# Optimization experiments

Hardware: AMD Instinct MI355X
Metric: run time of the kernel (lower is better)

Reference implementation:

```python
import jax, jax.numpy as jnp
import numpy as np

B, NPTS = 2, 60000
NX, NY = 256, 256
PCR0, PCR1 = -32.0, -32.0
PS0, PS1 = 0.25, 0.25
MAXPP = 32      # max points per pillar
MAXP = 12000    # max pillars
C = 64          # lidar_channels
SENT = NX * NY  # sentinel pillar id (> any valid id)
NEG = -1e9
EPS = 1e-5


def setup_inputs():
    key = jax.random.key(0)
    ks = jax.random.split(key, 16)
    xy = jax.random.uniform(ks[0], (B, NPTS, 2), minval=-34.0, maxval=34.0)
    z = jax.random.uniform(ks[1], (B, NPTS, 1), minval=-3.0, maxval=1.0)
    ir = jax.random.uniform(ks[2], (B, NPTS, 2))
    pts = jnp.concatenate([xy, z, ir], axis=-1).astype(jnp.float32)
    mask = jax.random.uniform(ks[3], (B, NPTS)) < 0.98

    def lin(k, i, o):
        return (jax.random.normal(k, (i, o)) / np.sqrt(i)).astype(jnp.float32)

    inp = {"lidar_points": pts, "lidar_mask": mask,
           "w1": lin(ks[4], 10, 64), "b1": 0.01 * jax.random.normal(ks[5], (64,), jnp.float32),
           "g1": jnp.ones(64, jnp.float32), "be1": jnp.zeros(64, jnp.float32),
           "w2": lin(ks[6], 64, 64), "b2": 0.01 * jax.random.normal(ks[7], (64,), jnp.float32),
           "g2": jnp.ones(64, jnp.float32), "be2": jnp.zeros(64, jnp.float32)}
    for i, n in enumerate(["1", "2", "3"]):
        inp["cw" + n] = (jax.random.normal(ks[8 + i], (64, 64, 3, 3)) / np.sqrt(64 * 9)).astype(jnp.float32)
        inp["cb" + n] = 0.01 * jax.random.normal(ks[11 + i], (64,), jnp.float32)
        inp["cg" + n] = jnp.ones(64, jnp.float32)
        inp["cbe" + n] = jnp.zeros(64, jnp.float32)
    return inp


def bn1d(x, g, b):  # training-mode BN over rows (biased var), matches torch BatchNorm1d forward
    m = x.mean(0)
    v = ((x - m) ** 2).mean(0)
    return (x - m) * jax.lax.rsqrt(v + EPS) * g + b


def bn2d(x, g, b):  # training-mode BN over (N,H,W) per channel
    m = x.mean((0, 2, 3), keepdims=True)
    v = ((x - m) ** 2).mean((0, 2, 3), keepdims=True)
    return (x - m) * jax.lax.rsqrt(v + EPS) * g[None, :, None, None] + b[None, :, None, None]


def conv3(x, w, b):
    y = jax.lax.conv_general_dilated(x, w, (1, 1), 'SAME',
                                     dimension_numbers=('NCHW', 'OIHW', 'NCHW'))
    return y + b[None, :, None, None]


def pillarize(pts, msk):
    """pts: (N,5) xyzir, msk: (N,) bool -> padded pillar tensors (fixed shapes)."""
    n = pts.shape[0]
    ix = jnp.clip(((pts[:, 0] - PCR0) / PS0).astype(jnp.int32), 0, NX - 1)
    iy = jnp.clip(((pts[:, 1] - PCR1) / PS1).astype(jnp.int32), 0, NY - 1)
    pid = jnp.where(msk, iy * NX + ix, SENT)
    # sorted unique ids; keep the first (smallest) MAXP, like torch.unique + truncation
    spid = jnp.sort(pid)
    is_new = jnp.concatenate([jnp.array([True]), spid[1:] != spid[:-1]])
    urank = jnp.cumsum(is_new) - 1
    dest = jnp.where(is_new & (urank < MAXP) & (spid < SENT), urank, MAXP)
    uids = jnp.full((MAXP + 1,), SENT, dtype=pid.dtype).at[dest].set(spid)[:MAXP]  # ascending, SENT-padded
    inv = jnp.clip(jnp.searchsorted(uids, pid), 0, MAXP - 1)
    valid = (uids[inv] == pid) & (pid < SENT)
    # rank of each point within its pillar, in original point order (stable sort)
    seg = jnp.where(valid, inv, MAXP)
    order = jnp.argsort(seg)  # stable
    sseg = seg[order]
    pos = jnp.arange(n)
    first = jnp.concatenate([jnp.array([True]), sseg[1:] != sseg[:-1]])
    start = jax.lax.cummax(jnp.where(first, pos, 0))
    rank = jnp.zeros(n, jnp.int32).at[order].set((pos - start).astype(jnp.int32))
    keep = valid & (rank < MAXPP)  # first MAXPP points per pillar (matches truncation-then-mean)
    seg2 = jnp.where(keep, inv, MAXP)  # dump slot = MAXP
    cnt = jnp.zeros(MAXP + 1, pts.dtype).at[seg2].add(1.0)
    sums = jnp.zeros((MAXP + 1, 3), pts.dtype).at[seg2].add(jnp.where(keep[:, None], pts[:, :3], 0.0))
    mean = sums / jnp.maximum(cnt, 1.0)[:, None]
    ctr = mean[seg2]  # per-point pillar centroid (over kept points)
    gx = PCR0 + ((pid % NX).astype(pts.dtype) + 0.5) * PS0
    gy = PCR1 + ((pid // NX).astype(pts.dtype) + 0.5) * PS1
    aug = jnp.concatenate([pts, pts[:, :3] - ctr, gx[:, None], gy[:, None]], axis=1)  # (N,10)
    rk = jnp.minimum(rank, MAXPP - 1)
    pf = jnp.zeros((MAXP + 1, MAXPP, 10), pts.dtype).at[seg2, rk].set(
        jnp.where(keep[:, None], aug, 0.0))[:MAXP]
    pm = jnp.zeros((MAXP + 1, MAXPP), bool).at[seg2, rk].set(keep)[:MAXP]
    pvalid = uids < SENT
    coords = jnp.where(pvalid[:, None], jnp.stack([uids % NX, uids // NX], axis=-1), 0)
    return pf, pm, coords, pvalid


def pillar_net(pf, pm, w1, b1, g1, be1, w2, b2, g2, be2):
    npil, pp, ci = pf.shape
    x = pf.reshape(npil * pp, ci) @ w1 + b1
    x = jax.nn.relu(bn1d(x, g1, be1))
    x = x @ w2 + b2
    x = jax.nn.relu(bn1d(x, g2, be2))
    x = x.reshape(npil, pp, -1)
    x = jnp.where(pm[:, :, None], x, NEG)
    return x.max(axis=1)  # (npil, C)


def reference(lidar_points, lidar_mask, w1, b1, g1, be1, w2, b2, g2, be2,
              cw1, cb1, cg1, cbe1, cw2, cb2, cg2, cbe2, cw3, cb3, cg3, cbe3):
    pf, pm, coords, pvalid = jax.vmap(pillarize)(lidar_points, lidar_mask)
    # pillar net is applied per batch element in the original loop -> per-sample BN stats
    feat = jax.vmap(lambda a, m: pillar_net(a, m, w1, b1, g1, be1, w2, b2, g2, be2))(pf, pm)
    lin = coords[..., 1] * NX + coords[..., 0]          # (B, MAXP)
    f = jnp.where(pvalid[..., None], feat, 0.0)          # padded pillars contribute nothing
    bev = jax.vmap(lambda l, ff: jnp.zeros((NY * NX, C), ff.dtype).at[l].add(ff))(lin, f)
    bev = bev.reshape(-1, NY, NX, C).transpose(0, 3, 1, 2)  # (B,C,NY,NX)
    x = jax.nn.relu(bn2d(conv3(bev, cw1, cb1), cg1, cbe1))
    x = jax.nn.relu(bn2d(conv3(x, cw2, cb2), cg2, cbe2))
    x = jax.nn.relu(bn2d(conv3(x, cw3, cb3), cg3, cbe3))
    return x
```

## Files before the change

### kernel.cpp

```cpp
#include <hip/hip_runtime.h>

#define NPTS 60000
#define NXG 256
#define NCELL 65536
#define MAXP 12000
#define MAXPP 32
#define NROWS (MAXP*MAXPP)

typedef float f32x32 __attribute__((ext_vector_type(32)));
typedef float f32x4  __attribute__((ext_vector_type(4)));
typedef short s16x8  __attribute__((ext_vector_type(8)));

__device__ __forceinline__ short to_bf16(float f){
  unsigned u = __float_as_uint(f);
  unsigned r = (u + 0x7FFFu + ((u>>16)&1u)) >> 16;
  return (short)r;
}

__global__ __launch_bounds__(256) void prep(uint4* __restrict__ p1, size_t n1,
                                            uint4* __restrict__ p2, size_t n2,
                                            const float* __restrict__ w0, const float* __restrict__ w1,
                                            const float* __restrict__ w2, short* __restrict__ wh,
                                            const float* __restrict__ mw1, const float* __restrict__ mw2,
                                            short* __restrict__ w1h, short* __restrict__ w2h){
  size_t idx = (size_t)blockIdx.x*256 + threadIdx.x;
  size_t stride = (size_t)gridDim.x*256;
  const uint4 z = make_uint4(0,0,0,0);
  for (size_t k=idx; k<n1; k+=stride) p1[k]=z;
  for (size_t k=idx; k<n2; k+=stride) p2[k]=z;
  for (size_t k=idx; k<3*36864; k+=stride){
    int l = (int)(k / 36864), r = (int)(k - (size_t)l*36864);
    const float* w = (l==0)? w0 : ((l==1)? w1 : w2);
    int ic = r & 63, oc = (r>>6)&63, tap = r>>12;
    wh[k] = to_bf16(w[(oc*64+ic)*9 + tap]);
  }
  for (size_t k=idx; k<2048; k+=stride){
    int kk = (int)(k>>6), oc = (int)(k&63);
    w1h[k] = (kk<10) ? to_bf16(mw1[kk*64+oc]) : (short)0;
  }
  for (size_t k=idx; k<4096; k+=stride)
    w2h[k] = to_bf16(mw2[k]);
}

__global__ void compute_pid(const float* __restrict__ pts, const void* __restrict__ maskp,
                            int* __restrict__ pid, int* __restrict__ pptr,
                            int* __restrict__ ccnt){
  __shared__ int cf32, cbig;
  if (threadIdx.x==0){ cf32=0; cbig=0; }
  __syncthreads();
  {
    int lf=0, lb=0;
    const unsigned* mu = (const unsigned*)maskp;
    for (int k=0;k<4;k++){
      unsigned x = mu[threadIdx.x*4+k];
      if (x==0x3f800000u) lf++;
      else if (x>1u) lb++;
    }
    if (lf) atomicAdd(&cf32, lf);
    if (lb) atomicAdd(&cbig, lb);
  }
  __syncthreads();
  int mode = (cf32>64) ? 2 : ((cbig>0) ? 1 : 0);
  int i = blockIdx.x*blockDim.x + threadIdx.x;
  if (i>=NPTS) return;
  int b = blockIdx.y;
  int gi = b*NPTS+i;
  bool m;
  if (mode==0)      m = ((const int*)maskp)[gi]!=0;
  else if (mode==1) m = ((const unsigned char*)maskp)[gi]!=0;
  else              m = ((const float*)maskp)[gi]!=0.f;
  int cell = -1;
  if (m){
    float x = pts[(size_t)gi*5+0], y = pts[(size_t)gi*5+1];
    int ix = (int)((x - (-32.0f)) / 0.25f);
    ix = ix<0?0:(ix>255?255:ix);
    int iy = (int)((y - (-32.0f)) / 0.25f);
    iy = iy<0?0:(iy>255?255:iy);
    cell = iy*NXG + ix;
    atomicAdd(&ccnt[b*NCELL+cell], 1);
  }
  pid[gi] = cell;
  pptr[gi] = -1;
}

__global__ __launch_bounds__(256) void scan_a(const int* __restrict__ ccnt,
                                              int2* __restrict__ bpart){
  int b = blockIdx.y, blk = blockIdx.x, t = threadIdx.x;
  int4 v = *(const int4*)&ccnt[b*NCELL + blk*1024 + t*4];
  int occ = (v.x>0)+(v.y>0)+(v.z>0)+(v.w>0);
  int cnt = v.x+v.y+v.z+v.w;
  #pragma unroll
  for (int off=32; off>0; off>>=1){
    occ += __shfl_xor(occ, off, 64);
    cnt += __shfl_xor(cnt, off, 64);
  }
  __shared__ int so[4], sc[4];
  int wv = t>>6, lane = t&63;
  if (lane==0){ so[wv]=occ; sc[wv]=cnt; }
  __syncthreads();
  if (t==0) bpart[b*64+blk] = make_int2(so[0]+so[1]+so[2]+so[3], sc[0]+sc[1]+sc[2]+sc[3]);
}

__global__ __launch_bounds__(256) void scan_b(const int* __restrict__ ccnt,
    const int2* __restrict__ bpart,
    int* __restrict__ crank, int* __restrict__ cstart, int* __restrict__ pcell,
    int* __restrict__ misc, int* __restrict__ heavy){
  __shared__ int swo[4], swc[4], sk[4];
  __shared__ int bo_, bc_;
  int b = blockIdx.y, blk = blockIdx.x, t = threadIdx.x;
  int wv = t>>6, lane = t&63;
  if (t < 64){
    int2 p = bpart[b*64+t];
    int po = (t<blk)? p.x : 0;
    int pc = (t<blk)? p.y : 0;
    int to = p.x;
    int tc = p.y;
    #pragma unroll
    for (int off=32; off>0; off>>=1){
      po += __shfl_xor(po, off, 64);
      pc += __shfl_xor(pc, off, 64);
      to += __shfl_xor(to, off, 64);
      tc += __shfl_xor(tc, off, 64);
    }
    if (t==0){
      bo_ = po; bc_ = pc;
      if (blk==0){
        misc[1+b] = (to < MAXP) ? to : MAXP;
        misc[5+b] = tc;
      }
    }
  }
  int4 v = *(const int4*)&ccnt[b*NCELL + blk*1024 + t*4];
  int occ = (v.x>0)+(v.y>0)+(v.z>0)+(v.w>0);
  int cnt = v.x+v.y+v.z+v.w;
  int io = occ, ic = cnt;
  #pragma unroll
  for (int off=1; off<64; off<<=1){
    int ao = __shfl_up(io, off, 64);
    int ac = __shfl_up(ic, off, 64);
    if (lane >= off){ io += ao; ic += ac; }
  }
  if (lane==63){ swo[wv]=io; swc[wv]=ic; }
  __syncthreads();
  int wvo=0, wvc=0;
  #pragma unroll
  for (int w2=0; w2<4; w2++){
    if (w2<wv){ wvo += swo[w2]; wvc += swc[w2]; }
  }
  int eo = bo_ + wvo + io - occ;
  int ec = bc_ + wvc + ic - cnt;
  int kept = 0;
  int cellb = blk*1024 + t*4;
  int vv[4] = {v.x,v.y,v.z,v.w};
  #pragma unroll
  for (int j=0;j<4;j++){
    int c = cellb+j; int val = vv[j];
    if (val>0){
      crank[b*NCELL+c]=eo; cstart[b*NCELL+c]=ec;
      if (eo<MAXP){
        pcell[b*MAXP+eo]=c;
        kept += (val<MAXPP)? val : MAXPP;
        if (val>MAXPP){
          int hi = atomicAdd(&heavy[b],1);
          if (hi<64) heavy[2 + b*64 + hi] = c;
        }
      }
      eo++; ec+=val;
    }
  }
  #pragma unroll
  for (int off=32; off>0; off>>=1) kept += __shfl_xor(kept, off, 64);
  if (lane==0) sk[wv]=kept;
  __syncthreads();
  if (t==0) atomicAdd(&misc[3+b], sk[0]+sk[1]+sk[2]+sk[3]);
}

__global__ void scatter_points(const int* __restrict__ pid, const int* __restrict__ ccnt,
    const int* __restrict__ crank, const int* __restrict__ cstart,
    int* __restrict__ ctmp, int* __restrict__ plist, int* __restrict__ pptr){
  int i = blockIdx.x*blockDim.x + threadIdx.x;
  if (i>=NPTS) return;
  int b = blockIdx.y;
  int gi = b*NPTS+i;
  int cell = pid[gi];
  if (cell<0) return;
  int bc = b*NCELL+cell;
  int pos = cstart[bc] + atomicAdd(&ctmp[bc],1);
  plist[b*NPTS+pos] = i;
  int r = crank[bc];
  if (r>=0 && r<MAXP && ccnt[bc]<=MAXPP) pptr[gi] = r;
}

__global__ void heavy_select(const int* __restrict__ ccnt, const int* __restrict__ crank,
    const int* __restrict__ cstart, const int* __restrict__ plist,
    const int* __restrict__ heavy, int* __restrict__ pptr){
  int b = blockIdx.y;
  int hn = heavy[b]; if (hn>64) hn=64;
  if ((int)blockIdx.x >= hn) return;
  int cell = heavy[2 + b*64 + blockIdx.x];
  int bc = b*NCELL+cell;
  int cnt = ccnt[bc], start = cstart[bc], pr = crank[bc];
  for (int e=threadIdx.x; e<cnt; e+=blockDim.x){
    int pe = plist[b*NPTS+start+e];
    int rank=0;
    for (int k=0;k<cnt;k++) rank += (plist[b*NPTS+start+k] < pe);
    if (rank<MAXPP) pptr[b*NPTS+pe] = pr;
  }
}

__global__ __launch_bounds__(256) void gather_cpts(const float* __restrict__ pts,
    const int* __restrict__ pid, const int* __restrict__ pptr,
    const int* __restrict__ plist, const int* __restrict__ misc,
    float* __restrict__ cpts, float* __restrict__ psum){
  int pos = blockIdx.x*256 + threadIdx.x;
  int b = blockIdx.y;
  if (pos >= misc[5+b]) return;
  int i = plist[b*NPTS+pos];
  int gi = b*NPTS+i;
  const float* qp = &pts[(size_t)gi*5];
  float x=qp[0], y=qp[1], z=qp[2], i1=qp[3], i2=qp[4];
  int cell = pid[gi];
  int rid = pptr[gi];
  float gx = -32.0f + ((float)(cell&255)+0.5f)*0.25f;
  float gy = -32.0f + ((float)(cell>>8)+0.5f)*0.25f;
  float4* cp = (float4*)&cpts[(size_t)(b*NPTS+pos)*8];
  cp[0] = make_float4(x,y,z,i1);
  cp[1] = make_float4(i2,gx,gy,__int_as_float(rid));
  if (rid>=0){
    float* s = &psum[(size_t)(b*MAXP+rid)*4];
    atomicAdd(s+0,x); atomicAdd(s+1,y); atomicAdd(s+2,z); atomicAdd(s+3,1.f);
  }
}

#define MM_ACC(K,V) { if ((K)<32) m0[(K)&31]+=(V); else if ((K)<64) m1[((K)-32)&31]+=(V); else m2+=(V); }
__global__ __launch_bounds__(256) void moments(const float* __restrict__ cpts,
    const float* __restrict__ psum, const int* __restrict__ misc,
    float* __restrict__ lstat){
  int b = blockIdx.y;
  int n = misc[5+b];
  f32x32 m0, m1; float m2 = 0.f;
  #pragma unroll
  for (int j=0;j<32;j++){ m0[j]=0.f; m1[j]=0.f; }
  for (int pos = blockIdx.x*256+threadIdx.x; pos<n; pos += gridDim.x*256){
    const float4* cp = (const float4*)&cpts[(size_t)(b*NPTS+pos)*8];
    float4 f1 = cp[0], f2 = cp[1];
    int rid = __float_as_int(f2.w);
    if (rid<0) continue;
    float4 mc = *(const float4*)&psum[(size_t)(b*MAXP+rid)*4];
    float inv = 1.f/fmaxf(mc.w,1.f);
    float aug[10] = {f1.x,f1.y,f1.z,f1.w,f2.x,
                     f1.x-mc.x*inv, f1.y-mc.y*inv, f1.z-mc.z*inv, f2.y, f2.z};
    #pragma unroll
    for (int d=0; d<10; d++){
      #pragma unroll
      for (int e=d; e<10; e++){
        const int k = d*10 - d*(d-1)/2 + (e-d);
        MM_ACC(k, aug[d]*aug[e]);
      }
      const int kl = 55+d;
      MM_ACC(kl, aug[d]);
    }
  }
  int lane = threadIdx.x & 63;
  int rep = ((blockIdx.x*256+threadIdx.x)>>6) & 15;
  float* dst = &lstat[(size_t)(rep*2+b)*65];
  #pragma unroll
  for (int j=0;j<32;j++){
    float v = m0[j];
    #pragma unroll
    for (int off=32; off>0; off>>=1) v += __shfl_xor(v, off, 64);
    if (lane==0) atomicAdd(&dst[j], v);
  }
  #pragma unroll
  for (int j=0;j<32;j++){
    float v = m1[j];
    #pragma unroll
    for (int off=32; off>0; off>>=1) v += __shfl_xor(v, off, 64);
    if (lane==0) atomicAdd(&dst[32+j], v);
  }
  {
    float v = m2;
    #pragma unroll
    for (int off=32; off>0; off>>=1) v += __shfl_xor(v, off, 64);
    if (lane==0) atomicAdd(&dst[64], v);
  }
}

#define MFMA16(A,B,C) __builtin_amdgcn_mfma_f32_16x16x32_bf16(A,B,C,0,0,0)

__global__ __launch_bounds__(256) void point_mlp(const float* __restrict__ cpts,
    const float* __restrict__ psum, const int* __restrict__ misc,
    const float* __restrict__ w1, const float* __restrict__ b1,
    const float* __restrict__ g1, const float* __restrict__ be1,
    const short* __restrict__ w1h, const short* __restrict__ w2h,
    const float* __restrict__ lstat, float* __restrict__ tbuf){
  __shared__ float sM[65];
  __shared__ float sBN1[128];
  __shared__ short zT[4][16*72];
  const int b = blockIdx.y;
  const int t = threadIdx.x;
  for (int e=t; e<65; e+=256){
    float s=0.f;
    for (int r=0;r<16;r++) s += lstat[(size_t)(r*2+b)*65+e];
    sM[e]=s;
  }
  __syncthreads();
  if (t < 64){
    int c = t;
    float wcol[10];
    #pragma unroll
    for (int d=0;d<10;d++) wcol[d] = w1[d*64+c];
    float b1c = b1[c];
    float nk = (float)misc[3+b];
    const float N = (float)NROWS;
    float pad = N - nk;
    float lw = 0.f;
    #pragma unroll
    for (int d=0;d<10;d++) lw += sM[55+d]*wcol[d];
    float s = nk*b1c + lw;
    float qq = nk*b1c*b1c + 2.f*b1c*lw;
    #pragma unroll
    for (int d=0; d<10; d++){
      #pragma unroll
      for (int e=d; e<10; e++){
        float m = sM[d*10 - d*(d-1)/2 + (e-d)];
        qq += ((d==e)?1.f:2.f)*m*wcol[d]*wcol[e];
      }
    }
    float St = s + pad*b1c;
    float Qt = qq + pad*b1c*b1c;
    float mu = St/N;
    float var = fmaxf(Qt/N - mu*mu, 0.f);
    float sc = g1[c]*rsqrtf(var+1e-5f);
    float sh = be1[c]-mu*sc;
    sBN1[c]=sc; sBN1[64+c]=b1c*sc+sh;
  }
  __syncthreads();
  const int lane = t & 63, wv = t >> 6;
  const int colx = lane & 15;
  const int kq = lane >> 4, kb = kq*8;
  s16x8 w1f0, w1f1, w1f2, w1f3;
  s16x8 a2f0, a2f1, a2f2, a2f3;
  s16x8 b2f0, b2f1, b2f2, b2f3;
  #pragma unroll
  for (int j=0;j<8;j++){
    w1f0[j]=w1h[(kb+j)*64 +  0+colx]; w1f1[j]=w1h[(kb+j)*64 + 16+colx];
    w1f2[j]=w1h[(kb+j)*64 + 32+colx]; w1f3[j]=w1h[(kb+j)*64 + 48+colx];
    a2f0[j]=w2h[(kb+j)*64 +  0+colx]; a2f1[j]=w2h[(kb+j)*64 + 16+colx];
    a2f2[j]=w2h[(kb+j)*64 + 32+colx]; a2f3[j]=w2h[(kb+j)*64 + 48+colx];
    b2f0[j]=w2h[(32+kb+j)*64 +  0+colx]; b2f1[j]=w2h[(32+kb+j)*64 + 16+colx];
    b2f2[j]=w2h[(32+kb+j)*64 + 32+colx]; b2f3[j]=w2h[(32+kb+j)*64 + 48+colx];
  }
  float sc1v0=sBN1[colx],    sh1v0=sBN1[64+colx];
  float sc1v1=sBN1[16+colx], sh1v1=sBN1[80+colx];
  float sc1v2=sBN1[32+colx], sh1v2=sBN1[96+colx];
  float sc1v3=sBN1[48+colx], sh1v3=sBN1[112+colx];
  const int n = misc[5+b];
  const int ntiles = (n+15)>>4;
  short* myZ = zT[wv];
  for (int tile = blockIdx.x*4 + wv; tile < ntiles; tile += gridDim.x*4){
    int pos0 = tile*16;
    int pos = pos0 + colx;
    float aug[10];
    #pragma unroll
    for (int d=0;d<10;d++) aug[d]=0.f;
    if (pos < n){
      const float4* cp = (const float4*)&cpts[(size_t)(b*NPTS+pos)*8];
      float4 f1 = cp[0], f2 = cp[1];
      int rid = __float_as_int(f2.w);
      int ridc = (rid>=0)? rid : 0;
      float4 mc = *(const float4*)&psum[(size_t)(b*MAXP+ridc)*4];
      float inv = 1.f/fmaxf(mc.w,1.f);
      aug[0]=f1.x; aug[1]=f1.y; aug[2]=f1.z; aug[3]=f1.w; aug[4]=f2.x;
      aug[5]=f1.x-mc.x*inv; aug[6]=f1.y-mc.y*inv; aug[7]=f1.z-mc.z*inv;
      aug[8]=f2.y; aug[9]=f2.z;
    }
    s16x8 af;
    #pragma unroll
    for (int j=0;j<8;j++){
      float v = 0.f;
      if (kq==0) v = aug[j];
      else if (kq==1 && j<2) v = aug[8+j];
      af[j] = to_bf16(v);
    }
    f32x4 y0={0.f,0.f,0.f,0.f}, y1=y0, y2=y0, y3=y0;
    y0 = MFMA16(af, w1f0, y0);
    y1 = MFMA16(af, w1f1, y1);
    y2 = MFMA16(af, w1f2, y2);
    y3 = MFMA16(af, w1f3, y3);
    #pragma unroll
    for (int m=0;m<4;m++){
      int pr = (kq*4+m)*72;
      myZ[pr +  0+colx] = to_bf16(fmaxf(y0[m]*sc1v0+sh1v0, 0.f));
      myZ[pr + 16+colx] = to_bf16(fmaxf(y1[m]*sc1v1+sh1v1, 0.f));
      myZ[pr + 32+colx] = to_bf16(fmaxf(y2[m]*sc1v2+sh1v2, 0.f));
      myZ[pr + 48+colx] = to_bf16(fmaxf(y3[m]*sc1v3+sh1v3, 0.f));
    }
    s16x8 az0 = *(const s16x8*)&myZ[colx*72 + kb];
    s16x8 az1 = *(const s16x8*)&myZ[colx*72 + 32 + kb];
    f32x4 t0={0.f,0.f,0.f,0.f}, t1=t0, t2=t0, t3=t0;
    t0 = MFMA16(az0, a2f0, t0); t0 = MFMA16(az1, b2f0, t0);
    t1 = MFMA16(az0, a2f1, t1); t1 = MFMA16(az1, b2f1, t1);
    t2 = MFMA16(az0, a2f2, t2); t2 = MFMA16(az1, b2f2, t2);
    t3 = MFMA16(az0, a2f3, t3); t3 = MFMA16(az1, b2f3, t3);
    #pragma unroll
    for (int m=0;m<4;m++){
      int pm = pos0 + kq*4 + m;
      if (pm < n){
        float* dst = &tbuf[(size_t)(b*NPTS+pm)*64];
        dst[ 0+colx] = t0[m];
        dst[16+colx] = t1[m];
        dst[32+colx] = t2[m];
        dst[48+colx] = t3[m];
      }
    }
  }
}

__global__ __launch_bounds__(256) void pillar_max(const float* __restrict__ tbuf,
    const float* __restrict__ cpts,
    const int* __restrict__ pcell, const int* __restrict__ cstart,
    const int* __restrict__ ccnt, const int* __restrict__ misc,
    float* __restrict__ l2stat, float* __restrict__ fmx, float* __restrict__ fmn){
  const int lane = threadIdx.x & 63;
  const int npil0 = misc[1], npil1 = misc[2];
  float s2_0=0.f, q2_0=0.f, s2_1=0.f, q2_1=0.f;
  const int wglobal = (blockIdx.x*256 + threadIdx.x) >> 6;
  const int nwaves = (gridDim.x*256) >> 6;
  for (int qq = wglobal; qq < 2*MAXP; qq += nwaves){
    int b = (qq >= MAXP) ? 1 : 0;
    int p = qq - b*MAXP;
    int npil = b ? npil1 : npil0;
    if (p >= npil) continue;
    int cell = pcell[b*MAXP+p];
    int bc = b*NCELL+cell;
    int cnt = ccnt[bc], start = cstart[bc];
    float tmax = -1e30f, tmin = 1e30f;
    float s2 = 0.f, q2 = 0.f;
    for (int k=0; k<cnt; k++){
      int rid = __float_as_int(cpts[(size_t)(b*NPTS+start+k)*8 + 7]);
      float tv = tbuf[(size_t)(b*NPTS+start+k)*64 + lane];
      if (rid == p){
        tmax = fmaxf(tmax, tv);
        tmin = fminf(tmin, tv);
        s2 += tv; q2 += tv*tv;
      }
    }
    fmx[(size_t)(b*MAXP+p)*64 + lane] = tmax;
    fmn[(size_t)(b*MAXP+p)*64 + lane] = tmin;
    if (b){ s2_1 += s2; q2_1 += q2; } else { s2_0 += s2; q2_0 += q2; }
  }
  int rep = wglobal & 15;
  atomicAdd(&l2stat[((rep*2+0)*2+0)*64+lane], s2_0);
  atomicAdd(&l2stat[((rep*2+0)*2+1)*64+lane], q2_0);
  atomicAdd(&l2stat[((rep*2+1)*2+0)*64+lane], s2_1);
  atomicAdd(&l2stat[((rep*2+1)*2+1)*64+lane], q2_1);
}

__global__ void stats_fin2(const float* __restrict__ w1, const float* __restrict__ b1,
    const float* __restrict__ g1, const float* __restrict__ be1,
    const float* __restrict__ w2, const float* __restrict__ b2,
    const float* __restrict__ g2, const float* __restrict__ be2,
    const float* __restrict__ lstat, const float* __restrict__ l2stat,
    const int* __restrict__ misc, float* __restrict__ stats){
  __shared__ float M[65];
  __shared__ float z0s[64];
  int b = blockIdx.x, c = threadIdx.x;
  for (int e=c; e<65; e+=64){
    float s=0.f;
    for (int r=0;r<16;r++) s += lstat[(size_t)(r*2+b)*65+e];
    M[e]=s;
  }
  __syncthreads();
  float wcol[10];
  #pragma unroll
  for (int d=0;d<10;d++) wcol[d] = w1[d*64+c];
  float b1c = b1[c];
  float nk = (float)misc[3+b];
  const float N = (float)NROWS;
  float pad = N - nk;
  float lw = 0.f;
  #pragma unroll
  for (int d=0;d<10;d++) lw += M[55+d]*wcol[d];
  float s = nk*b1c + lw;
  float qq = nk*b1c*b1c + 2.f*b1c*lw;
  #pragma unroll
  for (int d=0; d<10; d++){
    #pragma unroll
    for (int e=d; e<10; e++){
      float m = M[d*10 - d*(d-1)/2 + (e-d)];
      qq += ((d==e)?1.f:2.f)*m*wcol[d]*wcol[e];
    }
  }
  float St = s + pad*b1c;
  float Qt = qq + pad*b1c*b1c;
  float mu = St/N;
  float var = fmaxf(Qt/N - mu*mu, 0.f);
  float sc1 = g1[c]*rsqrtf(var+1e-5f);
  float sh1 = be1[c]-mu*sc1;
  float z0 = fmaxf(b1c*sc1+sh1, 0.f);
  z0s[c]=z0;
  __syncthreads();
  float t0 = b2[c];
  for (int i2=0;i2<64;i2++) t0 += z0s[i2]*w2[(size_t)i2*64+c];
  float s2 = pad*t0, q2 = pad*t0*t0;
  for (int r=0;r<16;r++){
    s2 += l2stat[((r*2+b)*2+0)*64+c];
    q2 += l2stat[((r*2+b)*2+1)*64+c];
  }
  float m2 = s2/N;
  float v2 = fmaxf(q2/N - m2*m2, 0.f);
  float sc2 = g2[c]*rsqrtf(v2+1e-5f);
  float* S = &stats[(size_t)b*512];
  S[384+c]=sc2; S[448+c]=be2[c]-m2*sc2;
}

__global__ void scatter_bev(const float* __restrict__ fmx, const float* __restrict__ fmn,
                            const int* __restrict__ pcell, const int* __restrict__ misc,
                            const float* __restrict__ stats, short* __restrict__ bevh){
  int tid = blockIdx.x*256+threadIdx.x;
  if (tid >= 2*64*MAXP) return;
  int c = tid & 63;
  int bp = tid >> 6;
  int b = bp / MAXP;
  int p = bp - b*MAXP;
  if (p >= misc[1+b]) return;
  float sc2 = stats[(size_t)b*512+384+c], sh2 = stats[(size_t)b*512+448+c];
  float t = (sc2 >= 0.f) ? fmx[tid] : fmn[tid];
  float v = fmaxf(sc2*t+sh2, 0.f);
  int cell = pcell[b*MAXP+p];
  bevh[((size_t)((b<<16) + cell))*64 + c] = to_bf16(v);
}

__global__ __launch_bounds__(512,4) void conv_mfma(const short* __restrict__ xh,
    const short* __restrict__ wh, const float* __restrict__ bias,
    const float* __restrict__ pstat, const float* __restrict__ pg, const float* __restrict__ pbe,
    short* __restrict__ outh, float* __restrict__ outf,
    float* __restrict__ stat){
  __shared__ short sX[324*40];
  __shared__ short sW[576*40];
  __shared__ float sBN[128];
  __shared__ float ss[64], sq[64];
  const int tX = blockIdx.x*16, tY = blockIdx.y*16;
  const int b = blockIdx.z;
  const int t = threadIdx.x;
  const int lane = t & 63, wv = t >> 6;
  const int colx = lane & 15;
  const int kb = (lane >> 4) * 8;
  const int ocb = (wv >> 2) * 32;
  const int ry  = (wv & 3) * 4;
  if (t < 64){ ss[t]=0.f; sq[t]=0.f; }
  if (t >= 64 && t < 128 && pstat){
    int c = t-64;
    const float n = 131072.f;
    float m = pstat[c]/n;
    float v = fmaxf(pstat[64+c]/n - m*m, 0.f);
    float sc = pg[c]*rsqrtf(v+1e-5f);
    sBN[c]=sc; sBN[64+c]=pbe[c]-m*sc;
  }

  f32x4 a00={0.f,0.f,0.f,0.f}, a01=a00, a02=a00, a03=a00;
  f32x4 a10=a00, a11=a00, a12=a00, a13=a00;

  for (int h=0; h<2; ++h){
    __syncthreads();
    for (int e=t; e<1296; e+=512){
      int px = e>>2, j = e&3;
      int yy = px/18, xx = px - yy*18;
      int gy = tY+yy-1, gx = tX+xx-1;
      uint4 v = make_uint4(0,0,0,0);
      if ((unsigned)gy<256u && (unsigned)gx<256u){
        v = *(const uint4*)&xh[((size_t)((b<<16) + (gy<<8) + gx))*64 + h*32 + j*8];
        if (pstat){
          unsigned arr[4] = {v.x, v.y, v.z, v.w};
          #pragma unroll
          for (int j2=0;j2<4;j2++){
            unsigned wrd = arr[j2];
            int ch = h*32 + j*8 + j2*2;
            float lo = __uint_as_float(wrd<<16);
            float hi = __uint_as_float(wrd & 0xffff0000u);
            lo = fmaxf(lo*sBN[ch]+sBN[64+ch], 0.f);
            hi = fmaxf(hi*sBN[ch+1]+sBN[64+ch+1], 0.f);
            arr[j2] = (unsigned)(unsigned short)to_bf16(lo) |
                      (((unsigned)(unsigned short)to_bf16(hi))<<16);
          }
          v = make_uint4(arr[0],arr[1],arr[2],arr[3]);
        }
      }
      *(uint4*)&sX[px*40 + j*8] = v;
    }
    for (int e=t; e<2304; e+=512){
      int row = e>>2, j = e&3;
      int tap = row>>6, oc = row&63;
      uint4 v = *(const uint4*)&wh[(size_t)tap*4096 + oc*64 + h*32 + j*8];
      *(uint4*)&sW[row*40 + j*8] = v;
    }
    __syncthreads();
    #pragma unroll
    for (int tap=0; tap<9; ++tap){
      const int dy = tap/3, dx = tap - dy*3;
      s16x8 wA = *(const s16x8*)&sW[(tap*64 + ocb +  0 + colx)*40 + kb];
      s16x8 wB = *(const s16x8*)&sW[(tap*64 + ocb + 16 + colx)*40 + kb];
      s16x8 x0 = *(const s16x8*)&sX[((ry+0+dy)*18 + colx+dx)*40 + kb];
      s16x8 x1 = *(const s16x8*)&sX[((ry+1+dy)*18 + colx+dx)*40 + kb];
      s16x8 x2 = *(const s16x8*)&sX[((ry+2+dy)*18 + colx+dx)*40 + kb];
      s16x8 x3 = *(const s16x8*)&sX[((ry+3+dy)*18 + colx+dx)*40 + kb];
      a00 = MFMA16(wA,x0,a00); a01 = MFMA16(wA,x1,a01);
      a02 = MFMA16(wA,x2,a02); a03 = MFMA16(wA,x3,a03);
      a10 = MFMA16(wB,x0,a10); a11 = MFMA16(wB,x1,a11);
      a12 = MFMA16(wB,x2,a12); a13 = MFMA16(wB,x3,a13);
    }
  }
  const int ocl = (lane>>4)*4;
  #define DOG(G, A0,A1,A2,A3) { \
    const int oc0g = ocb + G*16 + ocl; \
    float bj0=bias[oc0g], bj1=bias[oc0g+1], bj2=bias[oc0g+2], bj3=bias[oc0g+3]; \
    float v00=A0[0]+bj0, v01=A0[1]+bj1, v02=A0[2]+bj2, v03=A0[3]+bj3; \
    float v10=A1[0]+bj0, v11=A1[1]+bj1, v12=A1[2]+bj2, v13=A1[3]+bj3; \
    float v20=A2[0]+bj0, v21=A2[1]+bj1, v22=A2[2]+bj2, v23=A2[3]+bj3; \
    float v30=A3[0]+bj0, v31=A3[1]+bj1, v32=A3[2]+bj2, v33=A3[3]+bj3; \
    float s0=v00+v10+v20+v30, q0=v00*v00+v10*v10+v20*v20+v30*v30; \
    float s1=v01+v11+v21+v31, q1=v01*v01+v11*v11+v21*v21+v31*v31; \
    float s2=v02+v12+v22+v32, q2=v02*v02+v12*v12+v22*v22+v32*v32; \
    float s3=v03+v13+v23+v33, q3=v03*v03+v13*v13+v23*v23+v33*v33; \
    s0+=__shfl_xor(s0,1,64); s0+=__shfl_xor(s0,2,64); s0+=__shfl_xor(s0,4,64); s0+=__shfl_xor(s0,8,64); \
    q0+=__shfl_xor(q0,1,64); q0+=__shfl_xor(q0,2,64); q0+=__shfl_xor(q0,4,64); q0+=__shfl_xor(q0,8,64); \
    s1+=__shfl_xor(s1,1,64); s1+=__shfl_xor(s1,2,64); s1+=__shfl_xor(s1,4,64); s1+=__shfl_xor(s1,8,64); \
    q1+=__shfl_xor(q1,1,64); q1+=__shfl_xor(q1,2,64); q1+=__shfl_xor(q1,4,64); q1+=__shfl_xor(q1,8,64); \
    s2+=__shfl_xor(s2,1,64); s2+=__shfl_xor(s2,2,64); s2+=__shfl_xor(s2,4,64); s2+=__shfl_xor(s2,8,64); \
    q2+=__shfl_xor(q2,1,64); q2+=__shfl_xor(q2,2,64); q2+=__shfl_xor(q2,4,64); q2+=__shfl_xor(q2,8,64); \
    s3+=__shfl_xor(s3,1,64); s3+=__shfl_xor(s3,2,64); s3+=__shfl_xor(s3,4,64); s3+=__shfl_xor(s3,8,64); \
    q3+=__shfl_xor(q3,1,64); q3+=__shfl_xor(q3,2,64); q3+=__shfl_xor(q3,4,64); q3+=__shfl_xor(q3,8,64); \
    if (colx==0){ \
      atomicAdd(&ss[oc0g],s0);   atomicAdd(&sq[oc0g],q0); \
      atomicAdd(&ss[oc0g+1],s1); atomicAdd(&sq[oc0g+1],q1); \
      atomicAdd(&ss[oc0g+2],s2); atomicAdd(&sq[oc0g+2],q2); \
      atomicAdd(&ss[oc0g+3],s3); atomicAdd(&sq[oc0g+3],q3); \
    } \
    if (outh){ \
      size_t pb = (size_t)((b<<16) + tX + colx); \
      *(short4*)&outh[(pb + ((tY+ry+0)<<8))*64 + oc0g] = make_short4(to_bf16(v00),to_bf16(v01),to_bf16(v02),to_bf16(v03)); \
      *(short4*)&outh[(pb + ((tY+ry+1)<<8))*64 + oc0g] = make_short4(to_bf16(v10),to_bf16(v11),to_bf16(v12),to_bf16(v13)); \
      *(short4*)&outh[(pb + ((tY+ry+2)<<8))*64 + oc0g] = make_short4(to_bf16(v20),to_bf16(v21),to_bf16(v22),to_bf16(v23)); \
      *(short4*)&outh[(pb + ((tY+ry+3)<<8))*64 + oc0g] = make_short4(to_bf16(v30),to_bf16(v31),to_bf16(v32),to_bf16(v33)); \
    } else { \
      size_t cb0 = (((size_t)(b*64+oc0g))<<16) + ((tY+ry)<<8) + tX + colx; \
      outf[cb0          ] = v00; outf[cb0+(1<<16)      ] = v01; outf[cb0+(2<<16)      ] = v02; outf[cb0+(3<<16)      ] = v03; \
      outf[cb0+256      ] = v10; outf[cb0+(1<<16)+256  ] = v11; outf[cb0+(2<<16)+256  ] = v12; outf[cb0+(3<<16)+256  ] = v13; \
      outf[cb0+512      ] = v20; outf[cb0+(1<<16)+512  ] = v21; outf[cb0+(2<<16)+512  ] = v22; outf[cb0+(3<<16)+512  ] = v23; \
      outf[cb0+768      ] = v30; outf[cb0+(1<<16)+768  ] = v31; outf[cb0+(2<<16)+768  ] = v32; outf[cb0+(3<<16)+768  ] = v33; \
    } \
  }
  DOG(0, a00,a01,a02,a03)
  DOG(1, a10,a11,a12,a13)
  #undef DOG
  __syncthreads();
  if (t < 64){
    atomicAdd(&stat[t],    ss[t]);
    atomicAdd(&stat[64+t], sq[t]);
  }
}

__global__ __launch_bounds__(256) void bn_apply(float* __restrict__ x, const float* __restrict__ bnst,
                                                const float* __restrict__ g, const float* __restrict__ be){
  __shared__ float sBN[128];
  if (threadIdx.x < 64){
    int c = threadIdx.x;
    const float n = 131072.f;
    float m = bnst[c]/n;
    float v = fmaxf(bnst[64+c]/n - m*m, 0.f);
    float sc = g[c]*rsqrtf(v+1e-5f);
    sBN[c]=sc; sBN[64+c]=be[c]-m*sc;
  }
  __syncthreads();
  size_t idx = (size_t)blockIdx.x*256 + threadIdx.x;
  size_t stride = (size_t)gridDim.x*256;
  float4* p = (float4*)x;
  for (size_t k=idx; k<2097152ULL; k+=stride){
    int c = (int)((k>>14)&63);
    float sc = sBN[c], sh = sBN[64+c];
    float4 v = p[k];
    v.x=fmaxf(v.x*sc+sh,0.f); v.y=fmaxf(v.y*sc+sh,0.f);
    v.z=fmaxf(v.z*sc+sh,0.f); v.w=fmaxf(v.w*sc+sh,0.f);
    p[k]=v;
  }
}

extern "C" void kernel_launch(void* const* d_in, const int* in_sizes, int n_in,
                              void* d_out, int out_size, void* d_ws, size_t ws_size,
                              hipStream_t stream){
  const float* pts  = (const float*)d_in[0];
  const void*  mask = d_in[1];
  const float* w1 = (const float*)d_in[2];
  const float* b1 = (const float*)d_in[3];
  const float* g1 = (const float*)d_in[4];
  const float* be1= (const float*)d_in[5];
  const float* w2 = (const float*)d_in[6];
  const float* b2 = (const float*)d_in[7];
  const float* g2 = (const float*)d_in[8];
  const float* be2= (const float*)d_in[9];
  const float* cw[3]  = {(const float*)d_in[10],(const float*)d_in[14],(const float*)d_in[18]};
  const float* cb[3]  = {(const float*)d_in[11],(const float*)d_in[15],(const float*)d_in[19]};
  const float* cg[3]  = {(const float*)d_in[12],(const float*)d_in[16],(const float*)d_in[20]};
  const float* cbe[3] = {(const float*)d_in[13],(const float*)d_in[17],(const float*)d_in[21]};
  float* out = (float*)d_out;

  char* W = (char*)d_ws;
  size_t off = 0;
  auto A = [&](size_t n){ size_t r = off; off = (off + n + 255) & ~(size_t)255; return r; };
  short*    BIGH  = (short*)   (W + A((size_t)2*NCELL*64*2));
  short*    OUT1H = (short*)   (W + A((size_t)2*NCELL*64*2));
  int*      PID   = (int*)     (W + A((size_t)2*NPTS*4));
  int*      CRANK = (int*)     (W + A((size_t)2*NCELL*4));
  int*      CSTART= (int*)     (W + A((size_t)2*NCELL*4));
  int*      PLIST = (int*)     (W + A((size_t)2*NPTS*4));
  int*      PPTR  = (int*)     (W + A((size_t)2*NPTS*4));
  int*      PCELL = (int*)     (W + A((size_t)2*MAXP*4));
  float*    CPTS  = (float*)   (W + A((size_t)2*NPTS*8*4));
  float*    TBUF  = (float*)   (W + A((size_t)2*NPTS*64*4));
  float*    FMX   = (float*)   (W + A((size_t)2*MAXP*64*4));
  float*    FMN   = (float*)   (W + A((size_t)2*MAXP*64*4));
  short*    WH    = (short*)   (W + A((size_t)3*36864*2));
  short*    W1H   = (short*)   (W + A((size_t)2048*2));
  short*    W2H   = (short*)   (W + A((size_t)4096*2));
  int2*     BPART = (int2*)    (W + A((size_t)2*64*8));
  size_t zbeg = off;
  int*      CCNT  = (int*)     (W + A((size_t)2*NCELL*4));
  int*      CTMP  = (int*)     (W + A((size_t)2*NCELL*4));
  float*    PSUM  = (float*)   (W + A((size_t)2*MAXP*16));
  float*    STATS = (float*)   (W + A((size_t)2*512*4));
  float*    LSTAT = (float*)   (W + A((size_t)16*2*65*4));
  float*    L2STAT= (float*)   (W + A((size_t)16*2*2*64*4));
  float*    BNST  = (float*)   (W + A((size_t)3*256*4));
  int*      HEAVY = (int*)     (W + A((size_t)(2+2*64)*4));
  int*      MISC  = (int*)     (W + A(256));
  size_t zend = off;

  prep<<<2048,256,0,stream>>>((uint4*)BIGH, (size_t)2*NCELL*64*2/16,
                              (uint4*)(W+zbeg), (zend-zbeg)/16,
                              cw[0], cw[1], cw[2], WH, w1, w2, W1H, W2H);

  dim3 perPt((NPTS+255)/256, 2);

  compute_pid<<<perPt,256,0,stream>>>(pts, mask, PID, PPTR, CCNT);
  scan_a<<<dim3(64,2),256,0,stream>>>(CCNT, BPART);
  scan_b<<<dim3(64,2),256,0,stream>>>(CCNT, BPART, CRANK, CSTART, PCELL, MISC, HEAVY);
  scatter_points<<<perPt,256,0,stream>>>(PID, CCNT, CRANK, CSTART, CTMP, PLIST, PPTR);
  heavy_select<<<dim3(64,2),64,0,stream>>>(CCNT, CRANK, CSTART, PLIST, HEAVY, PPTR);
  gather_cpts<<<perPt,256,0,stream>>>(pts, PID, PPTR, PLIST, MISC, CPTS, PSUM);
  moments<<<dim3(120,2),256,0,stream>>>(CPTS, PSUM, MISC, LSTAT);
  point_mlp<<<dim3(128,2),256,0,stream>>>(CPTS, PSUM, MISC, w1, b1, g1, be1,
                                          W1H, W2H, LSTAT, TBUF);
  pillar_max<<<2048,256,0,stream>>>(TBUF, CPTS, PCELL, CSTART, CCNT, MISC,
                                    L2STAT, FMX, FMN);
  stats_fin2<<<2,64,0,stream>>>(w1, b1, g1, be1, w2, b2, g2, be2, LSTAT, L2STAT, MISC, STATS);
  scatter_bev<<<(2*64*MAXP+255)/256,256,0,stream>>>(FMX, FMN, PCELL, MISC, STATS, BIGH);

  conv_mfma<<<dim3(16,16,2),512,0,stream>>>(BIGH, WH, cb[0], nullptr, nullptr, nullptr,
                                            OUT1H, nullptr, BNST);
  conv_mfma<<<dim3(16,16,2),512,0,stream>>>(OUT1H, WH+36864, cb[1], BNST, cg[0], cbe[0],
                                            BIGH, nullptr, BNST+256);
  conv_mfma<<<dim3(16,16,2),512,0,stream>>>(BIGH, WH+2*36864, cb[2], BNST+256, cg[1], cbe[1],
                                            nullptr, out, BNST+512);
  bn_apply<<<2048,256,0,stream>>>(out, BNST+512, cg[2], cbe[2]);
}
```

Before: 230.7 us.

## Replace per-pillar max loop with segmented atomic max/min over sorted points

The pillar max/min reduction now walks fixed 16-point chunks of the sorted point list per wave and flushes each run with order-preserving unsigned atomicMax/atomicMin, instead of one wave per pillar looping over its cell's points. This spreads the work evenly across waves, where the old scheme gave each wave an uneven pillar load, and it drops the pcell/cstart/ccnt indirection. The cost is extra global atomics and an extra buffer initialisation. The moments kernel also stores the centered offsets into a widened cpts record so point_mlp no longer reads psum, and point_mlp's grid is doubled.

```diff
diff --git a/kernel.cpp b/kernel.cpp
--- a/kernel.cpp
+++ b/kernel.cpp
@@ -16,18 +16,29 @@
   unsigned r = (u + 0x7FFFu + ((u>>16)&1u)) >> 16;
   return (short)r;
 }
+__device__ __forceinline__ unsigned mapf(float f){
+  unsigned u = __float_as_uint(f);
+  return (u & 0x80000000u) ? ~u : (u | 0x80000000u);
+}
+__device__ __forceinline__ float unmapf(unsigned u){
+  unsigned b = (u & 0x80000000u) ? (u ^ 0x80000000u) : ~u;
+  return __uint_as_float(b);
+}
 
 __global__ __launch_bounds__(256) void prep(uint4* __restrict__ p1, size_t n1,
                                             uint4* __restrict__ p2, size_t n2,
                                             const float* __restrict__ w0, const float* __restrict__ w1,
                                             const float* __restrict__ w2, short* __restrict__ wh,
                                             const float* __restrict__ mw1, const float* __restrict__ mw2,
-                                            short* __restrict__ w1h, short* __restrict__ w2h){
+                                            short* __restrict__ w1h, short* __restrict__ w2h,
+                                            uint4* __restrict__ fmn, size_t nfmn){
   size_t idx = (size_t)blockIdx.x*256 + threadIdx.x;
   size_t stride = (size_t)gridDim.x*256;
   const uint4 z = make_uint4(0,0,0,0);
+  const uint4 ff = make_uint4(0xFFFFFFFFu,0xFFFFFFFFu,0xFFFFFFFFu,0xFFFFFFFFu);
   for (size_t k=idx; k<n1; k+=stride) p1[k]=z;
   for (size_t k=idx; k<n2; k+=stride) p2[k]=z;
+  for (size_t k=idx; k<nfmn; k+=stride) fmn[k]=ff;
   for (size_t k=idx; k<3*36864; k+=stride){
     int l = (int)(k / 36864), r = (int)(k - (size_t)l*36864);
     const float* w = (l==0)? w0 : ((l==1)? w1 : w2);
@@ -223,7 +234,7 @@
   int rid = pptr[gi];
   float gx = -32.0f + ((float)(cell&255)+0.5f)*0.25f;
   float gy = -32.0f + ((float)(cell>>8)+0.5f)*0.25f;
-  float4* cp = (float4*)&cpts[(size_t)(b*NPTS+pos)*8];
+  float4* cp = (float4*)&cpts[(size_t)(b*NPTS+pos)*12];
   cp[0] = make_float4(x,y,z,i1);
   cp[1] = make_float4(i2,gx,gy,__int_as_float(rid));
   if (rid>=0){
@@ -233,7 +244,7 @@
 }
 
 #define MM_ACC(K,V) { if ((K)<32) m0[(K)&31]+=(V); else if ((K)<64) m1[((K)-32)&31]+=(V); else m2+=(V); }
-__global__ __launch_bounds__(256) void moments(const float* __restrict__ cpts,
+__global__ __launch_bounds__(256) void moments(float* __restrict__ cpts,
     const float* __restrict__ psum, const int* __restrict__ misc,
     float* __restrict__ lstat){
   int b = blockIdx.y;
@@ -242,14 +253,15 @@
   #pragma unroll
   for (int j=0;j<32;j++){ m0[j]=0.f; m1[j]=0.f; }
   for (int pos = blockIdx.x*256+threadIdx.x; pos<n; pos += gridDim.x*256){
-    const float4* cp = (const float4*)&cpts[(size_t)(b*NPTS+pos)*8];
+    float4* cp = (float4*)&cpts[(size_t)(b*NPTS+pos)*12];
     float4 f1 = cp[0], f2 = cp[1];
     int rid = __float_as_int(f2.w);
     if (rid<0) continue;
     float4 mc = *(const float4*)&psum[(size_t)(b*MAXP+rid)*4];
     float inv = 1.f/fmaxf(mc.w,1.f);
-    float aug[10] = {f1.x,f1.y,f1.z,f1.w,f2.x,
-                     f1.x-mc.x*inv, f1.y-mc.y*inv, f1.z-mc.z*inv, f2.y, f2.z};
+    float dx = f1.x-mc.x*inv, dy = f1.y-mc.y*inv, dz = f1.z-mc.z*inv;
+    cp[2] = make_float4(dx,dy,dz,0.f);
+    float aug[10] = {f1.x,f1.y,f1.z,f1.w,f2.x, dx,dy,dz, f2.y,f2.z};
     #pragma unroll
     for (int d=0; d<10; d++){
       #pragma unroll
@@ -289,7 +301,7 @@
 #define MFMA16(A,B,C) __builtin_amdgcn_mfma_f32_16x16x32_bf16(A,B,C,0,0,0)
 
 __global__ __launch_bounds__(256) void point_mlp(const float* __restrict__ cpts,
-    const float* __restrict__ psum, const int* __restrict__ misc,
+    const int* __restrict__ misc,
     const float* __restrict__ w1, const float* __restrict__ b1,
     const float* __restrict__ g1, const float* __restrict__ be1,
     const short* __restrict__ w1h, const short* __restrict__ w2h,
@@ -365,14 +377,10 @@
     #pragma unroll
     for (int d=0;d<10;d++) aug[d]=0.f;
     if (pos < n){
-      const float4* cp = (const float4*)&cpts[(size_t)(b*NPTS+pos)*8];
-      float4 f1 = cp[0], f2 = cp[1];
-      int rid = __float_as_int(f2.w);
-      int ridc = (rid>=0)? rid : 0;
-      float4 mc = *(const float4*)&psum[(size_t)(b*MAXP+ridc)*4];
-      float inv = 1.f/fmaxf(mc.w,1.f);
+      const float4* cp = (const float4*)&cpts[(size_t)(b*NPTS+pos)*12];
+      float4 f1 = cp[0], f2 = cp[1], f3 = cp[2];
       aug[0]=f1.x; aug[1]=f1.y; aug[2]=f1.z; aug[3]=f1.w; aug[4]=f2.x;
-      aug[5]=f1.x-mc.x*inv; aug[6]=f1.y-mc.y*inv; aug[7]=f1.z-mc.z*inv;
+      aug[5]=f3.x; aug[6]=f3.y; aug[7]=f3.z;
       aug[8]=f2.y; aug[9]=f2.z;
     }
     s16x8 af;
@@ -417,44 +425,43 @@
   }
 }
 
-__global__ __launch_bounds__(256) void pillar_max(const float* __restrict__ tbuf,
-    const float* __restrict__ cpts,
-    const int* __restrict__ pcell, const int* __restrict__ cstart,
-    const int* __restrict__ ccnt, const int* __restrict__ misc,
-    float* __restrict__ l2stat, float* __restrict__ fmx, float* __restrict__ fmn){
+__global__ __launch_bounds__(256) void seg_max(const float* __restrict__ tbuf,
+    const float* __restrict__ cpts, const int* __restrict__ misc,
+    float* __restrict__ l2stat, unsigned* __restrict__ fmxU, unsigned* __restrict__ fmnU){
+  const int b = blockIdx.y;
   const int lane = threadIdx.x & 63;
-  const int npil0 = misc[1], npil1 = misc[2];
-  float s2_0=0.f, q2_0=0.f, s2_1=0.f, q2_1=0.f;
-  const int wglobal = (blockIdx.x*256 + threadIdx.x) >> 6;
-  const int nwaves = (gridDim.x*256) >> 6;
-  for (int qq = wglobal; qq < 2*MAXP; qq += nwaves){
-    int b = (qq >= MAXP) ? 1 : 0;
-    int p = qq - b*MAXP;
-    int npil = b ? npil1 : npil0;
-    if (p >= npil) continue;
-    int cell = pcell[b*MAXP+p];
-    int bc = b*NCELL+cell;
-    int cnt = ccnt[bc], start = cstart[bc];
+  const int n = misc[5+b];
+  const int w = blockIdx.x*4 + (threadIdx.x>>6);
+  float s2 = 0.f, q2 = 0.f;
+  int p0 = w*16;
+  if (p0 < n){
+    int p1 = p0+16; if (p1>n) p1=n;
+    int cur = -1;
     float tmax = -1e30f, tmin = 1e30f;
-    float s2 = 0.f, q2 = 0.f;
-    for (int k=0; k<cnt; k++){
-      int rid = __float_as_int(cpts[(size_t)(b*NPTS+start+k)*8 + 7]);
-      float tv = tbuf[(size_t)(b*NPTS+start+k)*64 + lane];
-      if (rid == p){
+    for (int pos=p0; pos<p1; ++pos){
+      int rid = __float_as_int(cpts[(size_t)(b*NPTS+pos)*12 + 7]);
+      float tv = tbuf[(size_t)(b*NPTS+pos)*64 + lane];
+      if (rid >= 0){
+        if (rid != cur){
+          if (cur >= 0){
+            atomicMax(&fmxU[(size_t)(b*MAXP+cur)*64 + lane], mapf(tmax));
+            atomicMin(&fmnU[(size_t)(b*MAXP+cur)*64 + lane], mapf(tmin));
+          }
+          cur = rid; tmax = -1e30f; tmin = 1e30f;
+        }
         tmax = fmaxf(tmax, tv);
         tmin = fminf(tmin, tv);
         s2 += tv; q2 += tv*tv;
       }
     }
-    fmx[(size_t)(b*MAXP+p)*64 + lane] = tmax;
-    fmn[(size_t)(b*MAXP+p)*64 + lane] = tmin;
-    if (b){ s2_1 += s2; q2_1 += q2; } else { s2_0 += s2; q2_0 += q2; }
-  }
-  int rep = wglobal & 15;
-  atomicAdd(&l2stat[((rep*2+0)*2+0)*64+lane], s2_0);
-  atomicAdd(&l2stat[((rep*2+0)*2+1)*64+lane], q2_0);
-  atomicAdd(&l2stat[((rep*2+1)*2+0)*64+lane], s2_1);
-  atomicAdd(&l2stat[((rep*2+1)*2+1)*64+lane], q2_1);
+    if (cur >= 0){
+      atomicMax(&fmxU[(size_t)(b*MAXP+cur)*64 + lane], mapf(tmax));
+      atomicMin(&fmnU[(size_t)(b*MAXP+cur)*64 + lane], mapf(tmin));
+    }
+  }
+  int rep = w & 15;
+  atomicAdd(&l2stat[((rep*2+b)*2+0)*64+lane], s2);
+  atomicAdd(&l2stat[((rep*2+b)*2+1)*64+lane], q2);
 }
 
 __global__ void stats_fin2(const float* __restrict__ w1, const float* __restrict__ b1,
@@ -515,7 +522,7 @@
   S[384+c]=sc2; S[448+c]=be2[c]-m2*sc2;
 }
 
-__global__ void scatter_bev(const float* __restrict__ fmx, const float* __restrict__ fmn,
+__global__ void scatter_bev(const unsigned* __restrict__ fmxU, const unsigned* __restrict__ fmnU,
                             const int* __restrict__ pcell, const int* __restrict__ misc,
                             const float* __restrict__ stats, short* __restrict__ bevh){
   int tid = blockIdx.x*256+threadIdx.x;
@@ -526,7 +533,7 @@
   int p = bp - b*MAXP;
   if (p >= misc[1+b]) return;
   float sc2 = stats[(size_t)b*512+384+c], sh2 = stats[(size_t)b*512+448+c];
-  float t = (sc2 >= 0.f) ? fmx[tid] : fmn[tid];
+  float t = (sc2 >= 0.f) ? unmapf(fmxU[tid]) : unmapf(fmnU[tid]);
   float v = fmaxf(sc2*t+sh2, 0.f);
   int cell = pcell[b*MAXP+p];
   bevh[((size_t)((b<<16) + cell))*64 + c] = to_bf16(v);
@@ -716,15 +723,15 @@
   int*      PLIST = (int*)     (W + A((size_t)2*NPTS*4));
   int*      PPTR  = (int*)     (W + A((size_t)2*NPTS*4));
   int*      PCELL = (int*)     (W + A((size_t)2*MAXP*4));
-  float*    CPTS  = (float*)   (W + A((size_t)2*NPTS*8*4));
+  float*    CPTS  = (float*)   (W + A((size_t)2*NPTS*12*4));
   float*    TBUF  = (float*)   (W + A((size_t)2*NPTS*64*4));
-  float*    FMX   = (float*)   (W + A((size_t)2*MAXP*64*4));
-  float*    FMN   = (float*)   (W + A((size_t)2*MAXP*64*4));
+  unsigned* FMN   = (unsigned*)(W + A((size_t)2*MAXP*64*4));
   short*    WH    = (short*)   (W + A((size_t)3*36864*2));
   short*    W1H   = (short*)   (W + A((size_t)2048*2));
   short*    W2H   = (short*)   (W + A((size_t)4096*2));
   int2*     BPART = (int2*)    (W + A((size_t)2*64*8));
   size_t zbeg = off;
+  unsigned* FMX   = (unsigned*)(W + A((size_t)2*MAXP*64*4));
   int*      CCNT  = (int*)     (W + A((size_t)2*NCELL*4));
   int*      CTMP  = (int*)     (W + A((size_t)2*NCELL*4));
   float*    PSUM  = (float*)   (W + A((size_t)2*MAXP*16));
@@ -738,7 +745,8 @@
 
   prep<<<2048,256,0,stream>>>((uint4*)BIGH, (size_t)2*NCELL*64*2/16,
                               (uint4*)(W+zbeg), (zend-zbeg)/16,
-                              cw[0], cw[1], cw[2], WH, w1, w2, W1H, W2H);
+                              cw[0], cw[1], cw[2], WH, w1, w2, W1H, W2H,
+                              (uint4*)FMN, (size_t)2*MAXP*64*4/16);
 
   dim3 perPt((NPTS+255)/256, 2);
 
@@ -749,10 +757,9 @@
   heavy_select<<<dim3(64,2),64,0,stream>>>(CCNT, CRANK, CSTART, PLIST, HEAVY, PPTR);
   gather_cpts<<<perPt,256,0,stream>>>(pts, PID, PPTR, PLIST, MISC, CPTS, PSUM);
   moments<<<dim3(120,2),256,0,stream>>>(CPTS, PSUM, MISC, LSTAT);
-  point_mlp<<<dim3(128,2),256,0,stream>>>(CPTS, PSUM, MISC, w1, b1, g1, be1,
+  point_mlp<<<dim3(256,2),256,0,stream>>>(CPTS, MISC, w1, b1, g1, be1,
                                           W1H, W2H, LSTAT, TBUF);
-  pillar_max<<<2048,256,0,stream>>>(TBUF, CPTS, PCELL, CSTART, CCNT, MISC,
-                                    L2STAT, FMX, FMN);
+  seg_max<<<dim3(938,2),256,0,stream>>>(TBUF, CPTS, MISC, L2STAT, FMX, FMN);
   stats_fin2<<<2,64,0,stream>>>(w1, b1, g1, be1, w2, b2, g2, be2, LSTAT, L2STAT, MISC, STATS);
   scatter_bev<<<(2*64*MAXP+255)/256,256,0,stream>>>(FMX, FMN, PCELL, MISC, STATS, BIGH);
 
```

After: 216.2 us. -6.3%, faster.
